# Kernel tuning notes

Hardware: AMD Instinct MI355X
Metric: run time of the kernel (lower is better)

## Reference

```python
import jax, jax.numpy as jnp
import numpy as np

B, S, H = 32, 256, 256
D = 2 * H          # BiLSTM output dim (hidden_dim*2)
F = 1024           # total fragment count across the batch
T = 5              # tagset size


def setup_inputs() -> dict:
    key = jax.random.key(0)
    ks = jax.random.split(key, 9)
    en_output = jax.random.normal(ks[0], (B, S, D), jnp.float32)
    # descending lengths, first sentence defines seq_length = S
    lengths = jnp.sort(jax.random.randint(ks[1], (B,), S // 2, S + 1))[::-1]
    lengths = lengths.at[0].set(S)
    frag_b = jax.random.randint(ks[2], (F,), 0, B)
    frag_s = jax.random.randint(ks[3], (F,), 0, S // 2 - 8)
    width = jax.random.randint(ks[4], (F,), 1, 8)
    frag_e = frag_s + width  # end exclusive, always <= lengths[frag_b]
    att_w = jax.random.normal(ks[5], (3 * D, D), jnp.float32) / np.float32(np.sqrt(3 * D))
    att_b = jax.random.normal(ks[6], (3 * D,), jnp.float32) * 0.01
    tag_w = jax.random.normal(ks[7], (T, 4 * D), jnp.float32) / np.float32(np.sqrt(4 * D))
    tag_b = jax.random.normal(ks[8], (T,), jnp.float32) * 0.01
    return {"en_output": en_output, "lengths": lengths, "frag_b": frag_b,
            "frag_s": frag_s, "frag_e": frag_e, "att_w": att_w, "att_b": att_b,
            "tag_w": tag_w, "tag_b": tag_b}


def reference(en_output, lengths, frag_b, frag_s, frag_e, att_w, att_b, tag_w, tag_b):
    Fn = frag_b.shape[0]
    Bn, Sn, Dn = en_output.shape
    dtype = en_output.dtype
    pos = jnp.arange(Sn)                                            # [S]
    in_span = (pos[None, :] >= frag_s[:, None]) & (pos[None, :] < frag_e[:, None])  # [F,S]
    memory = en_output[frag_b]                                      # [F,S,D] gather per fragment
    # word_state = sum of hidden states over the span (segment-sum via mask)
    word_state = jnp.einsum('fs,fsd->fd', in_span.astype(dtype), memory)
    l_word = en_output[frag_b, frag_s]                              # [F,D]
    r_word = en_output[frag_b, frag_e - 1]                          # [F,D]
    span = jnp.concatenate([l_word, word_state, r_word], axis=-1)   # [F,3D]
    # attention mask: the span itself and all padding positions are masked out
    att_mask = in_span | (pos[None, :] >= lengths[frag_b][:, None])  # [F,S]
    seq_len = lengths[0]
    # position distance (int), then position weight 1 - dist/seq_len
    pos_dis = jnp.where(pos[None, :] < frag_s[:, None], frag_s[:, None] - pos[None, :],
                jnp.where(pos[None, :] >= frag_e[:, None], pos[None, :] - frag_e[:, None] + 1,
                          seq_len)).astype(dtype)
    pos_weight = 1.0 - pos_dis / seq_len.astype(dtype)
    final = pos_weight[:, :, None] * memory                         # [F,S,D]
    # att(final) @ span == final @ (att_w.T span) + att_b.span ; att_w is [3D, D] (torch Linear weight)
    v = span @ att_w                                                # [F,D]
    c = span @ att_b                                                # [F]
    scores = jnp.tanh(jnp.einsum('fsd,fd->fs', final, v) + c[:, None])
    scores = jnp.where(att_mask, jnp.asarray(-1e4, dtype), scores)
    att = jax.nn.softmax(scores, axis=1)                            # [F,S]
    mix = jnp.einsum('fs,fsd->fd', att, final)                      # [F,D]
    mix_state = jnp.concatenate([span, mix], axis=-1)               # [F,4D]
    logits = mix_state @ tag_w.T + tag_b                            # [F,T]
    return jax.nn.log_softmax(logits, axis=1)
```

## Files before the change

### kernel.cpp

```cpp
#include <hip/hip_runtime.h>
#include <math.h>

#define BB 32
#define SS 256
#define DD 512
#define FF 1024
#define TT 5
#define K3 1536
#define K4 2048
#define GK 1536
#define SK 4
#define KCH (GK / SK)

__device__ __forceinline__ float wave_reduce_sum(float x) {
#pragma unroll
  for (int o = 32; o > 0; o >>= 1) x += __shfl_xor(x, o);
  return x;
}

__device__ __forceinline__ float fast_tanh(float x) {
  float ax = fabsf(x);
  float t = __expf(-2.f * ax);
  float r = (1.f - t) / (1.f + t);
  return x < 0.f ? -r : r;
}

__global__ __launch_bounds__(1024)
void bucket_kernel(const int* __restrict__ fb, int* __restrict__ order) {
  __shared__ int cnt[BB];
  __shared__ int start[BB];
  int t = threadIdx.x;
  if (t < BB) cnt[t] = 0;
  __syncthreads();
  int b = fb[t];
  int r = atomicAdd(&cnt[b], 1);
  __syncthreads();
  if (t == 0) {
    int acc = 0;
    for (int i = 0; i < BB; ++i) { start[i] = acc; acc += cnt[i]; }
  }
  __syncthreads();
  order[start[b] + r] = t;
}

__global__ __launch_bounds__(128)
void span_kernel(const float* __restrict__ en, const int* __restrict__ fb,
                 const int* __restrict__ fs, const int* __restrict__ fe,
                 const float* __restrict__ att_b, const int* __restrict__ order,
                 float* __restrict__ span, float* __restrict__ cvec)
{
  int bid = blockIdx.x;
  int f = order[(bid & 7) * (FF / 8) + (bid >> 3)];
  int t = threadIdx.x;
  int b = fb[f], s = fs[f], e = fe[f];
  const float* base = en + (size_t)b * SS * DD;
  int d0 = t * 4;
  float4 lw = *(const float4*)(base + (size_t)s * DD + d0);
  float4 rw = *(const float4*)(base + (size_t)(e - 1) * DD + d0);
  float4 wsum = make_float4(0.f, 0.f, 0.f, 0.f);
  for (int p = s; p < e; ++p) {
    float4 m = *(const float4*)(base + (size_t)p * DD + d0);
    wsum.x += m.x; wsum.y += m.y; wsum.z += m.z; wsum.w += m.w;
  }
  float* sp = span + (size_t)f * K3;
  *(float4*)(sp + d0) = lw;
  *(float4*)(sp + DD + d0) = wsum;
  *(float4*)(sp + 2 * DD + d0) = rw;
  float4 a0 = *(const float4*)(att_b + d0);
  float4 a1 = *(const float4*)(att_b + DD + d0);
  float4 a2 = *(const float4*)(att_b + 2 * DD + d0);
  float part = lw.x*a0.x + lw.y*a0.y + lw.z*a0.z + lw.w*a0.w
             + wsum.x*a1.x + wsum.y*a1.y + wsum.z*a1.z + wsum.w*a1.w
             + rw.x*a2.x + rw.y*a2.y + rw.z*a2.z + rw.w*a2.w;
  part = wave_reduce_sum(part);
  __shared__ float red[2];
  if ((t & 63) == 0) red[t >> 6] = part;
  __syncthreads();
  if (t == 0) cvec[f] = red[0] + red[1];
}

__global__ __launch_bounds__(256)
void gemm_v(const float* __restrict__ A,
            const float* __restrict__ Bw,
            float* __restrict__ Cpart)
{
  const int BM = 64, BN = 64, BK = 16;
  __shared__ float As[BK][BM + 4];
  __shared__ float Bs[BK][BN + 4];
  int t = threadIdx.x;
  int n0 = blockIdx.x * BN;
  int m0 = blockIdx.y * BM;
  int kbase = blockIdx.z * KCH;

  int ar = t >> 2;
  int ac = (t & 3) * 4;
  int br = t >> 4;
  int bc = (t & 15) * 4;
  int tm = (t >> 4) * 4;
  int tn = (t & 15) * 4;

  float acc[4][4] = {};

  for (int k0 = kbase; k0 < kbase + KCH; k0 += BK) {
    float4 av = *(const float4*)(A  + (size_t)(m0 + ar) * GK + k0 + ac);
    float4 bv = *(const float4*)(Bw + (size_t)(k0 + br) * DD + n0 + bc);
    __syncthreads();
    As[ac + 0][ar] = av.x;
    As[ac + 1][ar] = av.y;
    As[ac + 2][ar] = av.z;
    As[ac + 3][ar] = av.w;
    *(float4*)(&Bs[br][bc]) = bv;
    __syncthreads();
#pragma unroll
    for (int k = 0; k < BK; ++k) {
      float4 a = *(float4*)(&As[k][tm]);
      float4 b = *(float4*)(&Bs[k][tn]);
      acc[0][0] += a.x * b.x; acc[0][1] += a.x * b.y; acc[0][2] += a.x * b.z; acc[0][3] += a.x * b.w;
      acc[1][0] += a.y * b.x; acc[1][1] += a.y * b.y; acc[1][2] += a.y * b.z; acc[1][3] += a.y * b.w;
      acc[2][0] += a.z * b.x; acc[2][1] += a.z * b.y; acc[2][2] += a.z * b.z; acc[2][3] += a.z * b.w;
      acc[3][0] += a.w * b.x; acc[3][1] += a.w * b.y; acc[3][2] += a.w * b.z; acc[3][3] += a.w * b.w;
    }
  }
  float* Cp = Cpart + (size_t)blockIdx.z * FF * DD;
#pragma unroll
  for (int i = 0; i < 4; ++i) {
    *(float4*)(Cp + (size_t)(m0 + tm + i) * DD + n0 + tn) =
        make_float4(acc[i][0], acc[i][1], acc[i][2], acc[i][3]);
  }
}

__global__ __launch_bounds__(256)
void frag_kernel(const float* __restrict__ en, const int* __restrict__ lengths,
                 const int* __restrict__ fb, const int* __restrict__ fs,
                 const int* __restrict__ fe,
                 const float* __restrict__ span, const float* __restrict__ cvec,
                 const float* __restrict__ vpart,
                 const float* __restrict__ tag_w, const float* __restrict__ tag_b,
                 const int* __restrict__ order,
                 float* __restrict__ out)
{
  __shared__ float v_lds[DD];
  __shared__ float buf[4][DD];
  __shared__ float mstate[4][2];
  __shared__ float mix_lds[DD];
  __shared__ float pl[4 * TT];
  __shared__ float l5[TT];

  int bid = blockIdx.x;
  int f = order[(bid & 7) * (FF / 8) + (bid >> 3)];
  int t = threadIdx.x;
  int lane = t & 63, wv = t >> 6;
  int b = fb[f], s = fs[f], e = fe[f];
  int lenb = lengths[b];
  float seqlen = (float)lengths[0];
  float c = cvec[f];
  const float* mem = en + (size_t)b * SS * DD;

  if (t < 128) {
    float4 v0 = *(const float4*)(vpart + (size_t)f * DD + t * 4);
    float4 v1 = *(const float4*)(vpart + (size_t)FF * DD + (size_t)f * DD + t * 4);
    float4 v2 = *(const float4*)(vpart + 2 * (size_t)FF * DD + (size_t)f * DD + t * 4);
    float4 v3 = *(const float4*)(vpart + 3 * (size_t)FF * DD + (size_t)f * DD + t * 4);
    *(float4*)(v_lds + t * 4) = make_float4(v0.x + v1.x + v2.x + v3.x,
                                            v0.y + v1.y + v2.y + v3.y,
                                            v0.z + v1.z + v2.z + v3.z,
                                            v0.w + v1.w + v2.w + v3.w);
  }
  __syncthreads();

  float4 va = *(float4*)(v_lds + lane * 8);
  float4 vb = *(float4*)(v_lds + lane * 8 + 4);
  float m = -1e30f, ssum = 0.f;
  float am[8] = {0.f, 0.f, 0.f, 0.f, 0.f, 0.f, 0.f, 0.f};

  int rows = lenb - wv * 64;
  if (rows > 64) rows = 64;
  for (int i0 = 0; i0 < rows; i0 += 8) {
    float4 R0[8], R1[8];
    float d8[8];
#pragma unroll
    for (int k = 0; k < 8; ++k) {
      if (i0 + k < rows) {
        int p = wv * 64 + i0 + k;
        const float* row = mem + (size_t)p * DD + lane * 8;
        R0[k] = *(const float4*)(row);
        R1[k] = *(const float4*)(row + 4);
        d8[k] = R0[k].x*va.x + R0[k].y*va.y + R0[k].z*va.z + R0[k].w*va.w
              + R1[k].x*vb.x + R1[k].y*vb.y + R1[k].z*vb.z + R1[k].w*vb.w;
      } else {
        d8[k] = 0.f;
      }
    }
#pragma unroll
    for (int o = 32; o > 0; o >>= 1) {
#pragma unroll
      for (int k = 0; k < 8; ++k) d8[k] += __shfl_xor(d8[k], o);
    }
#pragma unroll
    for (int k = 0; k < 8; ++k) {
      int p = wv * 64 + i0 + k;
      bool live = (i0 + k < rows) && !(p >= s && p < e);
      if (live) {
        float dis = (p < s) ? (float)(s - p) : (float)(p - e + 1);
        float pw = 1.f - dis / seqlen;
        float sc = fast_tanh(pw * d8[k] + c);
        if (sc > m) {
          float scale = __expf(m - sc);
          ssum *= scale;
#pragma unroll
          for (int j = 0; j < 8; ++j) am[j] *= scale;
          m = sc;
        }
        float u = __expf(sc - m);
        ssum += u;
        float upw = u * pw;
        am[0] += upw * R0[k].x; am[1] += upw * R0[k].y; am[2] += upw * R0[k].z; am[3] += upw * R0[k].w;
        am[4] += upw * R1[k].x; am[5] += upw * R1[k].y; am[6] += upw * R1[k].z; am[7] += upw * R1[k].w;
      }
    }
  }
  if (lane == 0) { mstate[wv][0] = m; mstate[wv][1] = ssum; }
  __syncthreads();
  float M = fmaxf(fmaxf(mstate[0][0], mstate[1][0]), fmaxf(mstate[2][0], mstate[3][0]));
  float S = mstate[0][1] * __expf(mstate[0][0] - M)
          + mstate[1][1] * __expf(mstate[1][0] - M)
          + mstate[2][1] * __expf(mstate[2][0] - M)
          + mstate[3][1] * __expf(mstate[3][0] - M);
  float ew = __expf(m - M);
  {
    float4 s0 = make_float4(am[0] * ew, am[1] * ew, am[2] * ew, am[3] * ew);
    float4 s1 = make_float4(am[4] * ew, am[5] * ew, am[6] * ew, am[7] * ew);
    *(float4*)(&buf[wv][lane * 8]) = s0;
    *(float4*)(&buf[wv][lane * 8 + 4]) = s1;
  }
  __syncthreads();
  {
    int d0 = t * 2;
    float inv = 1.f / S;
    mix_lds[d0]     = (buf[0][d0] + buf[1][d0] + buf[2][d0] + buf[3][d0]) * inv;
    mix_lds[d0 + 1] = (buf[0][d0 + 1] + buf[1][d0 + 1] + buf[2][d0 + 1] + buf[3][d0 + 1]) * inv;
  }
  __syncthreads();

  float vals[8];
  int idx = t * 8;
  if (idx < K3) {
    const float* sp = span + (size_t)f * K3 + idx;
    float4 x0 = *(const float4*)(sp);
    float4 x1 = *(const float4*)(sp + 4);
    vals[0]=x0.x; vals[1]=x0.y; vals[2]=x0.z; vals[3]=x0.w;
    vals[4]=x1.x; vals[5]=x1.y; vals[6]=x1.z; vals[7]=x1.w;
  } else {
#pragma unroll
    for (int j = 0; j < 8; ++j) vals[j] = mix_lds[idx - K3 + j];
  }
  float acc5[TT];
#pragma unroll
  for (int tg = 0; tg < TT; ++tg) {
    const float* twr = tag_w + (size_t)tg * K4 + idx;
    float a = 0.f;
#pragma unroll
    for (int j = 0; j < 8; ++j) a += vals[j] * twr[j];
    acc5[tg] = wave_reduce_sum(a);
  }
  if (lane == 0) {
#pragma unroll
    for (int tg = 0; tg < TT; ++tg) pl[wv * TT + tg] = acc5[tg];
  }
  __syncthreads();
  if (t < TT) {
    l5[t] = pl[t] + pl[TT + t] + pl[2 * TT + t] + pl[3 * TT + t] + tag_b[t];
  }
  __syncthreads();
  if (t == 0) {
    float mm = l5[0];
#pragma unroll
    for (int j = 1; j < TT; ++j) mm = fmaxf(mm, l5[j]);
    float se = 0.f;
#pragma unroll
    for (int j = 0; j < TT; ++j) se += __expf(l5[j] - mm);
    float lse = mm + logf(se);
#pragma unroll
    for (int j = 0; j < TT; ++j) out[(size_t)f * TT + j] = l5[j] - lse;
  }
}

extern "C" void kernel_launch(void* const* d_in, const int* in_sizes, int n_in,
                              void* d_out, int out_size, void* d_ws, size_t ws_size,
                              hipStream_t stream) {
  const float* en      = (const float*)d_in[0];
  const int*   lengths = (const int*)d_in[1];
  const int*   frag_b  = (const int*)d_in[2];
  const int*   frag_s  = (const int*)d_in[3];
  const int*   frag_e  = (const int*)d_in[4];
  const float* att_w   = (const float*)d_in[5];
  const float* att_b   = (const float*)d_in[6];
  const float* tag_w   = (const float*)d_in[7];
  const float* tag_b   = (const float*)d_in[8];
  float* out = (float*)d_out;

  float* span  = (float*)d_ws;
  float* cvec  = span + (size_t)FF * K3;
  float* vpart = cvec + FF;
  int*   order = (int*)(vpart + (size_t)SK * FF * DD);

  bucket_kernel<<<1, FF, 0, stream>>>(frag_b, order);
  span_kernel<<<FF, 128, 0, stream>>>(en, frag_b, frag_s, frag_e, att_b, order, span, cvec);
  gemm_v<<<dim3(8, 16, SK), 256, 0, stream>>>(span, att_w, vpart);
  frag_kernel<<<FF, 256, 0, stream>>>(en, lengths, frag_b, frag_s, frag_e,
                                      span, cvec, vpart, tag_w, tag_b, order, out);
}
```

Measured before the change: 156.2 us.

## Use fixed softmax max from tanh bound and prefetch GEMM tiles into registers

The attention softmax drops the running max and rescaling, because tanh keeps scores in [-1,1] and so a fixed shift of 1 is safe. This removes the per-row branch, the rescale of the 8 accumulators, and one barrier plus the cross-wave max merge. The v GEMM now loads the next K tile into registers before computing on the current one, so global loads overlap with the FMA work. The division by seqlen is replaced by a multiply with a precomputed reciprocal. Masked rows still contribute zero, and the fixed shift only holds because scores are bounded.

```diff
diff --git a/kernel.cpp b/kernel.cpp
--- a/kernel.cpp
+++ b/kernel.cpp
@@ -85,6 +85,7 @@
             float* __restrict__ Cpart)
 {
   const int BM = 64, BN = 64, BK = 16;
+  const int NIT = KCH / BK;
   __shared__ float As[BK][BM + 4];
   __shared__ float Bs[BK][BN + 4];
   int t = threadIdx.x;
@@ -101,9 +102,13 @@
 
   float acc[4][4] = {};
 
-  for (int k0 = kbase; k0 < kbase + KCH; k0 += BK) {
-    float4 av = *(const float4*)(A  + (size_t)(m0 + ar) * GK + k0 + ac);
-    float4 bv = *(const float4*)(Bw + (size_t)(k0 + br) * DD + n0 + bc);
+  const float* Aptr = A  + (size_t)(m0 + ar) * GK + kbase + ac;
+  const float* Bptr = Bw + (size_t)(kbase + br) * DD + n0 + bc;
+
+  float4 av = *(const float4*)(Aptr);
+  float4 bv = *(const float4*)(Bptr);
+
+  for (int it = 0; it < NIT; ++it) {
     __syncthreads();
     As[ac + 0][ar] = av.x;
     As[ac + 1][ar] = av.y;
@@ -111,6 +116,10 @@
     As[ac + 3][ar] = av.w;
     *(float4*)(&Bs[br][bc]) = bv;
     __syncthreads();
+    if (it + 1 < NIT) {
+      av = *(const float4*)(Aptr + (it + 1) * BK);
+      bv = *(const float4*)(Bptr + (size_t)(it + 1) * BK * DD);
+    }
 #pragma unroll
     for (int k = 0; k < BK; ++k) {
       float4 a = *(float4*)(&As[k][tm]);
@@ -141,7 +150,7 @@
 {
   __shared__ float v_lds[DD];
   __shared__ float buf[4][DD];
-  __shared__ float mstate[4][2];
+  __shared__ float wsum[4];
   __shared__ float mix_lds[DD];
   __shared__ float pl[4 * TT];
   __shared__ float l5[TT];
@@ -153,6 +162,7 @@
   int b = fb[f], s = fs[f], e = fe[f];
   int lenb = lengths[b];
   float seqlen = (float)lengths[0];
+  float invseq = 1.f / seqlen;
   float c = cvec[f];
   const float* mem = en + (size_t)b * SS * DD;
 
@@ -170,7 +180,7 @@
 
   float4 va = *(float4*)(v_lds + lane * 8);
   float4 vb = *(float4*)(v_lds + lane * 8 + 4);
-  float m = -1e30f, ssum = 0.f;
+  float ssum = 0.f;
   float am[8] = {0.f, 0.f, 0.f, 0.f, 0.f, 0.f, 0.f, 0.f};
 
   int rows = lenb - wv * 64;
@@ -202,16 +212,9 @@
       bool live = (i0 + k < rows) && !(p >= s && p < e);
       if (live) {
         float dis = (p < s) ? (float)(s - p) : (float)(p - e + 1);
-        float pw = 1.f - dis / seqlen;
+        float pw = 1.f - dis * invseq;
         float sc = fast_tanh(pw * d8[k] + c);
-        if (sc > m) {
-          float scale = __expf(m - sc);
-          ssum *= scale;
-#pragma unroll
-          for (int j = 0; j < 8; ++j) am[j] *= scale;
-          m = sc;
-        }
-        float u = __expf(sc - m);
+        float u = __expf(sc - 1.f);
         ssum += u;
         float upw = u * pw;
         am[0] += upw * R0[k].x; am[1] += upw * R0[k].y; am[2] += upw * R0[k].z; am[3] += upw * R0[k].w;
@@ -219,24 +222,14 @@
       }
     }
   }
-  if (lane == 0) { mstate[wv][0] = m; mstate[wv][1] = ssum; }
-  __syncthreads();
-  float M = fmaxf(fmaxf(mstate[0][0], mstate[1][0]), fmaxf(mstate[2][0], mstate[3][0]));
-  float S = mstate[0][1] * __expf(mstate[0][0] - M)
-          + mstate[1][1] * __expf(mstate[1][0] - M)
-          + mstate[2][1] * __expf(mstate[2][0] - M)
-          + mstate[3][1] * __expf(mstate[3][0] - M);
-  float ew = __expf(m - M);
+  if (lane == 0) wsum[wv] = ssum;
+  *(float4*)(&buf[wv][lane * 8])     = make_float4(am[0], am[1], am[2], am[3]);
+  *(float4*)(&buf[wv][lane * 8 + 4]) = make_float4(am[4], am[5], am[6], am[7]);
+  __syncthreads();
   {
-    float4 s0 = make_float4(am[0] * ew, am[1] * ew, am[2] * ew, am[3] * ew);
-    float4 s1 = make_float4(am[4] * ew, am[5] * ew, am[6] * ew, am[7] * ew);
-    *(float4*)(&buf[wv][lane * 8]) = s0;
-    *(float4*)(&buf[wv][lane * 8 + 4]) = s1;
-  }
-  __syncthreads();
-  {
+    float S = wsum[0] + wsum[1] + wsum[2] + wsum[3];
+    float inv = 1.f / S;
     int d0 = t * 2;
-    float inv = 1.f / S;
     mix_lds[d0]     = (buf[0][d0] + buf[1][d0] + buf[2][d0] + buf[3][d0]) * inv;
     mix_lds[d0 + 1] = (buf[0][d0 + 1] + buf[1][d0 + 1] + buf[2][d0 + 1] + buf[3][d0 + 1]) * inv;
   }
```

New measurement: 149.9 us. -4.1%, faster.
